# Performance work log

Hardware: AMD Instinct MI355X
Metric: run time of the kernel (lower is better)

## Reference

```python
import jax, jax.numpy as jnp
import numpy as np
from jax import lax

B, N, NPOINT, NSAMPLE = 8, 8192, 1024, 32
IN_CH = 64
MLP = [128, 128, 256]
EPS = 1e-5  # BatchNorm eps (inference mode with running stats)


def setup_inputs() -> dict:
    key = jax.random.key(0)
    ks = jax.random.split(key, 2 + len(MLP))
    inp = {
        "xyz": jax.random.normal(ks[0], (B, N, 3), jnp.float32),
        "feature": jax.random.normal(ks[1], (B, IN_CH, N), jnp.float32),
    }
    last = IN_CH
    for li, out in enumerate(MLP):
        k = jax.random.split(ks[2 + li], 3)
        inp[f"w{li}"] = jax.random.normal(k[0], (out, last), jnp.float32) / np.sqrt(last).astype(np.float32)
        inp[f"b{li}"] = jnp.zeros((out,), jnp.float32)
        inp[f"gamma{li}"] = jnp.ones((out,), jnp.float32)
        inp[f"beta{li}"] = jnp.zeros((out,), jnp.float32)
        inp[f"mean{li}"] = 0.1 * jax.random.normal(k[1], (out,), jnp.float32)
        inp[f"var{li}"] = 1.0 + 0.1 * jax.random.uniform(k[2], (out,), jnp.float32)
        last = out
    return inp


def furthest_point_sample(xyz, npoint):
    # xyz: [B, N, 3] -> idx [B, npoint] (sequential FPS via scan)
    Bn, Nn, _ = xyz.shape
    start = jnp.zeros((Bn,), jnp.int32)

    def step(carry, _):
        mind, last = carry
        p = jnp.take_along_axis(xyz, last[:, None, None], axis=1)  # [B,1,3]
        d = jnp.sum((xyz - p) ** 2, axis=-1)  # [B,N]
        mind = jnp.minimum(mind, d)
        nxt = jnp.argmax(mind, axis=-1).astype(jnp.int32)
        return (mind, nxt), nxt

    init = (jnp.full((Bn, Nn), 1e10, xyz.dtype), start)
    _, rest = lax.scan(step, init, None, length=npoint - 1)  # [npoint-1, B]
    return jnp.concatenate([start[None, :], rest], axis=0).T  # [B, npoint]


def k_neighbor_query(new_xyz, xyz, k):
    # squared distances via ||a||^2 + ||b||^2 - 2 a.b  (no [B,S,N,3] blowup)
    d = (jnp.sum(new_xyz ** 2, -1)[:, :, None]
         + jnp.sum(xyz ** 2, -1)[:, None, :]
         - 2.0 * jnp.einsum('bsc,bnc->bsn', new_xyz, xyz))  # [B,S,N]
    _, idx = lax.top_k(-d, k)  # k smallest distances
    return idx  # [B,S,k]


def _mlp_layers(x, params):
    # x: [B, Cin, S, k]; each layer: 1x1 conv -> BN (running stats) -> ReLU
    for (w, b, g, bt, m, v) in params:
        y = jnp.einsum('oi,bisk->bosk', w, x) + b[None, :, None, None]
        inv = (g / jnp.sqrt(v + EPS))[None, :, None, None]
        x = jax.nn.relu((y - m[None, :, None, None]) * inv + bt[None, :, None, None])
    return x


def reference(xyz, feature,
              w0, b0, gamma0, beta0, mean0, var0,
              w1, b1, gamma1, beta1, mean1, var1,
              w2, b2, gamma2, beta2, mean2, var2):
    idx = furthest_point_sample(xyz, NPOINT)                     # [B,S]
    new_xyz = jnp.take_along_axis(xyz, idx[:, :, None], axis=1)  # [B,S,3]
    nidx = k_neighbor_query(new_xyz, xyz, NSAMPLE)               # [B,S,k]
    # grouping_operation: gather neighbor features -> [B,D,S,k]
    grouped = jax.vmap(lambda f, i: f[:, i])(feature, nidx)
    params = [(w0, b0, gamma0, beta0, mean0, var0),
              (w1, b1, gamma1, beta1, mean1, var1),
              (w2, b2, gamma2, beta2, mean2, var2)]
    x = _mlp_layers(grouped, params)
    new_feature = jnp.max(x, axis=3)  # [B, D', S]
    return new_xyz, new_feature
```

## Files before the change

kernel.cpp:

```cpp
#include <hip/hip_runtime.h>
#include <hip/hip_bf16.h>
#include <math.h>

#define B_  8
#define N_  8192
#define S_  1024
#define K_  32
#define C0_ 64
#define NK  184
#define NM  64
#define NP_KNN 23
#define BINS 2048
#define CCAP 256

typedef __attribute__((ext_vector_type(8))) short short8;
typedef __attribute__((ext_vector_type(4))) float f32x4;
typedef __attribute__((ext_vector_type(2))) float f32x2;

#define WH_OFF    0
#define WL_OFF    114688
#define SC_OFF    229376
#define SH_OFF    231424
#define FT_OFF    233472
#define NIDX2_OFF 8622080
#define SLOT_OFF  10719232
#define FLAG_OFF  10915840
#define WL0E 0
#define WL1E 8192
#define WL2E 24576
#define FLAG_MAGIC(w) (0x5AB00000u | (unsigned)(w))

__device__ __forceinline__ void split_bf16(float x, unsigned short& h, unsigned short& l) {
    __hip_bfloat16 hb = __float2bfloat16(x);
    float hf = __bfloat162float(hb);
    __hip_bfloat16 lb = __float2bfloat16(x - hf);
    h = *(unsigned short*)&hb;
    l = *(unsigned short*)&lb;
}

__device__ __forceinline__ f32x4 mfma16(short8 a, short8 b, f32x4 c) {
    return __builtin_amdgcn_mfma_f32_16x16x32_bf16(a, b, c, 0, 0, 0);
}

template<int CTRL, int RMASK>
__device__ __forceinline__ unsigned long long dpp_max_step(unsigned long long k) {
    unsigned lo = (unsigned)k, hi = (unsigned)(k >> 32);
    unsigned tlo = (unsigned)__builtin_amdgcn_update_dpp(0, (int)lo, CTRL, RMASK, 0xF, false);
    unsigned thi = (unsigned)__builtin_amdgcn_update_dpp(0, (int)hi, CTRL, RMASK, 0xF, false);
    unsigned long long t = ((unsigned long long)thi << 32) | (unsigned long long)tlo;
    return (t > k) ? t : k;
}
__device__ __forceinline__ unsigned long long wave_max_u64(unsigned long long k) {
    k = dpp_max_step<0x111, 0xF>(k);
    k = dpp_max_step<0x112, 0xF>(k);
    k = dpp_max_step<0x114, 0xF>(k);
    k = dpp_max_step<0x118, 0xF>(k);
    k = dpp_max_step<0x142, 0xA>(k);
    k = dpp_max_step<0x143, 0xC>(k);
    return k;
}
__device__ __forceinline__ unsigned long long umax64(unsigned long long a, unsigned long long b) {
    return (a > b) ? a : b;
}

__device__ __forceinline__ void block_sync_lds() {
    asm volatile("" ::: "memory");
    __builtin_amdgcn_s_waitcnt(0xC07F);
    __builtin_amdgcn_s_barrier();
    asm volatile("" ::: "memory");
}

struct KnnSh {
    unsigned hist[2][BINS];
    unsigned long long cand[2][CCAP];
    unsigned long long kslots[2][2][4];
    int sel[2][K_];
    unsigned wpart[2][4];
    int sBin[2], sBelow[2];
    unsigned cnt_sel[2], cnt_cand[2];
    int fallback;
    float qpt[2][4];
};

template<int AF, int KC, bool LAST>
__device__ __forceinline__ void layer(
    const unsigned short* __restrict__ Xin, int rsi,
    unsigned short* __restrict__ Xout,
    const unsigned short* __restrict__ Wh, const unsigned short* __restrict__ Wl,
    const float* __restrict__ sc, const float* __restrict__ sh,
    float* __restrict__ outg, int wid, int ln15, int quad)
{
    const int K = KC * 32;
    f32x4 acc[AF][8];
    #pragma unroll
    for (int a = 0; a < AF; ++a)
        #pragma unroll
        for (int j = 0; j < 8; ++j) acc[a][j] = (f32x4){0.f, 0.f, 0.f, 0.f};

    #pragma unroll
    for (int kc = 0; kc < KC; ++kc) {
        const int k0 = kc * 32 + quad * 8;
        short8 bf[8];
        #pragma unroll
        for (int j = 0; j < 8; ++j)
            bf[j] = *(const short8*)(Xin + (j * 16 + ln15) * rsi + k0);
        #pragma unroll
        for (int a = 0; a < AF; ++a) {
            const int row = wid * (AF * 16) + a * 16 + ln15;
            short8 ah = *(const short8*)(Wh + (size_t)row * K + k0);
            short8 al = *(const short8*)(Wl + (size_t)row * K + k0);
            #pragma unroll
            for (int j = 0; j < 8; ++j) {
                acc[a][j] = mfma16(al, bf[j], acc[a][j]);
                acc[a][j] = mfma16(ah, bf[j], acc[a][j]);
            }
        }
    }
    #pragma unroll
    for (int a = 0; a < AF; ++a) {
        const int o4 = wid * (AF * 16) + a * 16 + quad * 4;
        f32x4 scv = *(const f32x4*)(sc + o4);
        f32x4 shv = *(const f32x4*)(sh + o4);
        if (LAST) {
            #pragma unroll
            for (int qq = 0; qq < 4; ++qq) {
                float m4[4];
                #pragma unroll
                for (int r = 0; r < 4; ++r) {
                    float v0 = fmaxf(acc[a][2 * qq][r]     * scv[r] + shv[r], 0.f);
                    float v1 = fmaxf(acc[a][2 * qq + 1][r] * scv[r] + shv[r], 0.f);
                    float mm = fmaxf(v0, v1);
                    mm = fmaxf(mm, __shfl_xor(mm, 1));
                    mm = fmaxf(mm, __shfl_xor(mm, 2));
                    mm = fmaxf(mm, __shfl_xor(mm, 4));
                    mm = fmaxf(mm, __shfl_xor(mm, 8));
                    m4[r] = mm;
                }
                if (ln15 == 0) {
                    #pragma unroll
                    for (int r = 0; r < 4; ++r)
                        outg[(size_t)(o4 + r) * S_ + qq] = m4[r];
                }
            }
        } else {
            #pragma unroll
            for (int j = 0; j < 8; ++j) {
                unsigned short pq[4];
                #pragma unroll
                for (int r = 0; r < 4; ++r) {
                    float v = fmaxf(acc[a][j][r] * scv[r] + shv[r], 0.f);
                    __hip_bfloat16 hb = __float2bfloat16(v);
                    pq[r] = *(unsigned short*)&hb;
                }
                *(unsigned long long*)(Xout + (j * 16 + ln15) * 136 + o4) = *(unsigned long long*)pq;
            }
        }
    }
}

__global__ __launch_bounds__(512, 2) void fused_kernel(
    const float* __restrict__ xyz, const float* __restrict__ feature,
    const float* __restrict__ w0, const float* __restrict__ w1, const float* __restrict__ w2,
    const float* __restrict__ b0, const float* __restrict__ g0, const float* __restrict__ be0,
    const float* __restrict__ m0, const float* __restrict__ v0,
    const float* __restrict__ b1, const float* __restrict__ g1, const float* __restrict__ be1,
    const float* __restrict__ m1, const float* __restrict__ v1,
    const float* __restrict__ b2, const float* __restrict__ g2, const float* __restrict__ be2,
    const float* __restrict__ m2, const float* __restrict__ v2,
    char* __restrict__ ws, float* __restrict__ out)
{
    __shared__ __align__(16) char smraw[131584];
    const int tid = threadIdx.x;
    const int bid = (int)blockIdx.x;

    if (bid < B_) {
        #pragma clang fp contract(off)
        const int b = bid;
        float4* xyzw = (float4*)smraw;
        unsigned long long* wredA = (unsigned long long*)(smraw + N_ * 16);
        unsigned long long* wredB = wredA + 8;
        unsigned long long* slots = (unsigned long long*)(ws + SLOT_OFF) + (size_t)b * S_ * 3;

        f32x2 px[8], py[8], pz[8], mind[8];
        const float* xb = xyz + (size_t)b * N_ * 3;
        #pragma unroll
        for (int j = 0; j < 8; ++j) {
            int n0 = (2 * j) * 512 + tid, n1 = n0 + 512;
            float x0 = xb[n0 * 3], y0 = xb[n0 * 3 + 1], z0 = xb[n0 * 3 + 2];
            float x1 = xb[n1 * 3], y1 = xb[n1 * 3 + 1], z1 = xb[n1 * 3 + 2];
            px[j] = (f32x2){x0, x1}; py[j] = (f32x2){y0, y1}; pz[j] = (f32x2){z0, z1};
            xyzw[n0] = make_float4(x0, y0, z0, 0.f);
            xyzw[n1] = make_float4(x1, y1, z1, 0.f);
            mind[j] = (f32x2){1e10f, 1e10f};
        }
        __syncthreads();

        float4 p0 = xyzw[0];
        float lx = p0.x, ly = p0.y, lz = p0.z;
        if (tid < 3) {
            float v = (tid == 0) ? lx : ((tid == 1) ? ly : lz);
            __hip_atomic_store(slots + tid, (unsigned long long)__float_as_uint(v),
                               __ATOMIC_RELAXED, __HIP_MEMORY_SCOPE_AGENT);
        }
        const int lane = tid & 63, wid = tid >> 6;

        for (int it = 1; it < S_; ++it) {
            f32x2 lx2 = (f32x2){lx, lx}, ly2 = (f32x2){ly, ly}, lz2 = (f32x2){lz, lz};
            float bv = -1.0f; int bj = 0;
            #pragma unroll
            for (int j = 0; j < 8; ++j) {
                f32x2 dx = px[j] - lx2;
                f32x2 dy = py[j] - ly2;
                f32x2 dz = pz[j] - lz2;
                f32x2 t = dx * dx;
                t = t + dy * dy;
                t = t + dz * dz;
                f32x2 mv = mind[j];
                float m0v = fminf(mv.x, t.x);
                float m1v = fminf(mv.y, t.y);
                mind[j] = (f32x2){m0v, m1v};
                if (m0v > bv) { bv = m0v; bj = 2 * j; }
                if (m1v > bv) { bv = m1v; bj = 2 * j + 1; }
            }
            unsigned long long key =
                ((unsigned long long)__float_as_uint(bv) << 32) |
                (unsigned long long)(0xFFFFFFFFu - (unsigned)(bj * 512 + tid));
            key = wave_max_u64(key);
            unsigned long long* wred = (it & 1) ? wredA : wredB;
            if (lane == 63) wred[wid] = key;
            block_sync_lds();
            unsigned long long g0v = umax64(wred[0], wred[1]);
            unsigned long long g1v = umax64(wred[2], wred[3]);
            unsigned long long g2v = umax64(wred[4], wred[5]);
            unsigned long long g3v = umax64(wred[6], wred[7]);
            unsigned long long g = umax64(umax64(g0v, g1v), umax64(g2v, g3v));
            int ns = (int)(0xFFFFFFFFu - (unsigned)(g & 0xFFFFFFFFull));
            float4 p = xyzw[ns];
            lx = p.x; ly = p.y; lz = p.z;
            if (tid < 3) {
                float v = (tid == 0) ? lx : ((tid == 1) ? ly : lz);
                __hip_atomic_store(slots + (size_t)it * 3 + tid,
                                   (((unsigned long long)(unsigned)it) << 32) | __float_as_uint(v),
                                   __ATOMIC_RELAXED, __HIP_MEMORY_SCOPE_AGENT);
            }
        }
        return;
    }

    if (bid < B_ + NK) {
        const int w = bid - B_;

        {
            unsigned short* th = (unsigned short*)smraw;
            for (int t = w; t < 1024; t += NK) {
                int bb = t >> 7, n0 = (t & 127) * 64;
                __syncthreads();
                {
                    int cg = tid >> 6, ln = tid & 63;
                    const float* fb = feature + (size_t)bb * C0_ * N_;
                    #pragma unroll
                    for (int i = 0; i < 8; ++i) {
                        int c = cg * 8 + i;
                        __hip_bfloat16 hb = __float2bfloat16(fb[(size_t)c * N_ + n0 + ln]);
                        th[ln * 72 + c] = *(unsigned short*)&hb;
                    }
                }
                __syncthreads();
                {
                    int n = tid >> 3, c0 = (tid & 7) * 8;
                    unsigned short* ft = (unsigned short*)(ws + FT_OFF) + ((size_t)(bb * N_ + n0 + n)) * C0_ + c0;
                    *(short8*)ft = *(const short8*)(th + n * 72 + c0);
                }
            }
        }
        if (w < 112) {
            int i = w * 512 + tid;
            float x;
            if (i < WL1E)      x = w0[i];
            else if (i < WL2E) x = w1[i - WL1E];
            else               x = w2[i - WL2E];
            unsigned short h, l;
            split_bf16(x, h, l);
            ((unsigned short*)(ws + WH_OFF))[i] = h;
            ((unsigned short*)(ws + WL_OFF))[i] = l;
        } else if (w == 112) {
            int o = tid;
            if (o < 512) {
                const float *bb_, *gg, *be_, *mm, *vv; int oo;
                if (o < 128)      { bb_ = b0; gg = g0; be_ = be0; mm = m0; vv = v0; oo = o; }
                else if (o < 256) { bb_ = b1; gg = g1; be_ = be1; mm = m1; vv = v1; oo = o - 128; }
                else              { bb_ = b2; gg = g2; be_ = be2; mm = m2; vv = v2; oo = o - 256; }
                float scv = gg[oo] / sqrtf(vv[oo] + 1e-5f);
                ((float*)(ws + SC_OFF))[o] = scv;
                ((float*)(ws + SH_OFF))[o] = (bb_[oo] - mm[oo]) * scv + be_[oo];
            }
        }
        __syncthreads();
        if (tid == 0)
            __hip_atomic_store((unsigned*)(ws + FLAG_OFF) + w, FLAG_MAGIC(w),
                               __ATOMIC_RELEASE, __HIP_MEMORY_SCOPE_AGENT);

        KnnSh* S = (KnnSh*)smraw;
        const int ht = tid & 255, half = tid >> 8;
        const int lane = tid & 63, widH = (tid >> 6) & 3;
        unsigned long long* nidx2 = (unsigned long long*)(ws + NIDX2_OFF);
        const unsigned long long* slots = (const unsigned long long*)(ws + SLOT_OFF);

        for (int p = 0; p < NP_KNN; ++p) {
            int qA = p * (NK * 2) + w * 2;
            int q = qA + half;
            bool active = q < B_ * S_;
            int qc = active ? q : (B_ * S_ - 1);
            int s = qc >> 3, bq = qc & 7;

            if (tid == 0) {
                #pragma unroll
                for (int h = 0; h < 2; ++h) {
                    int qq = qA + h;
                    if (qq >= B_ * S_) continue;
                    int ss = qq >> 3, bb = qq & 7;
                    const unsigned long long* sl = slots + ((size_t)bb * S_ + ss) * 3;
                    #pragma unroll
                    for (int c = 0; c < 3; ++c) {
                        unsigned long long v;
                        for (;;) {
                            v = __hip_atomic_load(sl + c, __ATOMIC_RELAXED, __HIP_MEMORY_SCOPE_AGENT);
                            if ((int)(v >> 32) == ss) break;
                            __builtin_amdgcn_s_sleep(8);
                        }
                        S->qpt[h][c] = __uint_as_float((unsigned)v);
                    }
                }
            }
            __syncthreads();

            if (active && ht < 3) out[(size_t)(bq * S_ + s) * 3 + ht] = S->qpt[half][ht];

            #pragma unroll
            for (int i = 0; i < BINS / 256; ++i) S->hist[half][ht + i * 256] = 0;
            if (ht == 0) { S->cnt_sel[half] = 0; S->cnt_cand[half] = 0; if (tid == 0) S->fallback = 0; }

            float qx = S->qpt[half][0], qy = S->qpt[half][1], qz = S->qpt[half][2];
            float sa = __fadd_rn(__fadd_rn(__fmul_rn(qx, qx), __fmul_rn(qy, qy)), __fmul_rn(qz, qz));

            unsigned key[32];
            const float* base = xyz + (size_t)bq * N_ * 3;
            #pragma unroll
            for (int i = 0; i < 32; ++i) {
                int n = i * 256 + ht;
                float x = base[n * 3], y = base[n * 3 + 1], z = base[n * 3 + 2];
                float sb  = __fadd_rn(__fadd_rn(__fmul_rn(x, x), __fmul_rn(y, y)), __fmul_rn(z, z));
                float dot = __fadd_rn(__fadd_rn(__fmul_rn(qx, x), __fmul_rn(qy, y)), __fmul_rn(qz, z));
                float d   = __fsub_rn(__fadd_rn(sa, sb), __fmul_rn(2.0f, dot));
                unsigned u = __float_as_uint(d);
                key[i] = u ^ (unsigned)(((int)u >> 31) | (int)0x80000000);
            }
            __syncthreads();
            if (active) {
                #pragma unroll
                for (int i = 0; i < 32; ++i) atomicAdd(&S->hist[half][key[i] >> 21], 1u);
            }
            __syncthreads();

            unsigned h8[8], lsum = 0;
            #pragma unroll
            for (int i = 0; i < 8; ++i) { h8[i] = S->hist[half][ht * 8 + i]; lsum += h8[i]; }
            unsigned inc = lsum;
            #pragma unroll
            for (int off = 1; off < 64; off <<= 1) {
                unsigned o = __shfl_up(inc, off);
                if (lane >= off) inc += o;
            }
            if (lane == 63) S->wpart[half][widH] = inc;
            __syncthreads();
            unsigned basec = 0;
            #pragma unroll
            for (int w4 = 0; w4 < 4; ++w4) if (w4 < widH) basec += S->wpart[half][w4];
            unsigned excl = basec + inc - lsum;
            if (active && excl < (unsigned)K_ && excl + lsum >= (unsigned)K_) {
                unsigned c = excl;
                #pragma unroll
                for (int i = 0; i < 8; ++i) {
                    if (c < (unsigned)K_ && c + h8[i] >= (unsigned)K_) { S->sBin[half] = ht * 8 + i; S->sBelow[half] = (int)c; }
                    c += h8[i];
                }
            }
            __syncthreads();
            const unsigned Bbin = (unsigned)S->sBin[half];
            const int below = S->sBelow[half];

            if (active) {
                #pragma unroll
                for (int i = 0; i < 32; ++i) {
                    unsigned bin = key[i] >> 21;
                    int n = i * 256 + ht;
                    if (bin < Bbin) {
                        unsigned pp = atomicAdd(&S->cnt_sel[half], 1u);
                        if (pp < (unsigned)K_) S->sel[half][pp] = n;
                    } else if (bin == Bbin) {
                        unsigned pp = atomicAdd(&S->cnt_cand[half], 1u);
                        if (pp < CCAP) S->cand[half][pp] = ((unsigned long long)key[i] << 32) | (unsigned)n;
                    }
                }
            }
            __syncthreads();
            int m = (int)S->cnt_cand[half];
            if (active && ht == 0 && m > CCAP) S->fallback = 1;
            __syncthreads();

            if (!S->fallback) {
                if (widH == 0) {
                    int mtake = active ? (K_ - below) : 0;
                    if (mtake < 0) mtake = 0; if (mtake > K_) mtake = K_;
                    int mm = active ? m : 0;
                    unsigned long long v[4];
                    #pragma unroll
                    for (int j = 0; j < 4; ++j) {
                        int pp = lane + j * 64;
                        v[j] = (pp < mm) ? S->cand[half][pp] : ~0ull;
                    }
                    for (int r = 0; r < mtake; ++r) {
                        unsigned long long loc = v[0];
                        #pragma unroll
                        for (int j = 1; j < 4; ++j) if (v[j] < loc) loc = v[j];
                        unsigned long long g = loc;
                        #pragma unroll
                        for (int off = 1; off < 64; off <<= 1) {
                            unsigned long long o = __shfl_xor(g, off);
                            if (o < g) g = o;
                        }
                        #pragma unroll
                        for (int j = 0; j < 4; ++j) if (v[j] == g) v[j] = ~0ull;
                        if (lane == 0) S->sel[half][below + r] = (int)(unsigned)(g & 0xFFFFFFFFull);
                    }
                }
                __syncthreads();
            } else {
                unsigned bk = 0xFFFFFFFFu; int bi = 0;
                #pragma unroll
                for (int i = 0; i < 32; ++i) if (key[i] < bk) { bk = key[i]; bi = i; }
                for (int r = 0; r < K_; ++r) {
                    unsigned long long pk = ((unsigned long long)bk << 32) | (unsigned)(bi * 256 + ht);
                    #pragma unroll
                    for (int off = 1; off < 64; off <<= 1) {
                        unsigned long long o = __shfl_xor(pk, off);
                        if (o < pk) pk = o;
                    }
                    if (lane == 0) S->kslots[half][r & 1][widH] = pk;
                    __syncthreads();
                    unsigned long long g = S->kslots[half][r & 1][0];
                    #pragma unroll
                    for (int w4 = 1; w4 < 4; ++w4) { unsigned long long o = S->kslots[half][r & 1][w4]; if (o < g) g = o; }
                    int wn = (int)(unsigned)(g & 0xFFFFFFFFull);
                    if (ht == 0) S->sel[half][r] = wn;
                    if ((wn & 255) == ht) {
                        int iw = wn >> 8;
                        #pragma unroll
                        for (int ii = 0; ii < 32; ++ii) if (ii == iw) key[ii] = 0xFFFFFFFFu;
                        bk = 0xFFFFFFFFu; bi = 0;
                        #pragma unroll
                        for (int ii = 0; ii < 32; ++ii) if (key[ii] < bk) { bk = key[ii]; bi = ii; }
                    }
                }
                __syncthreads();
            }
            if (active && ht < K_)
                __hip_atomic_store(nidx2 + (size_t)q * K_ + ht,
                                   (((unsigned long long)(unsigned)q) << 32) | (unsigned)S->sel[half][ht],
                                   __ATOMIC_RELAXED, __HIP_MEMORY_SCOPE_AGENT);
            __syncthreads();
        }
        return;
    }

    {
        const int m = bid - B_ - NK;
        const int ht = tid & 255;
        const int lane = tid & 63, widH = (tid >> 6) & 3;
        const int ln15 = lane & 15, quad = lane >> 4;

        unsigned short* XA = (unsigned short*)smraw;
        unsigned short* XB = (unsigned short*)(smraw + 34816);
        int* nid = (int*)(smraw + 69632);

        {
            volatile unsigned* fl = (volatile unsigned*)(ws + FLAG_OFF);
            if (tid < NK) {
                while (__hip_atomic_load((const unsigned*)(ws + FLAG_OFF) + tid,
                                         __ATOMIC_RELAXED, __HIP_MEMORY_SCOPE_AGENT) != FLAG_MAGIC(tid))
                    __builtin_amdgcn_s_sleep(16);
            }
            (void)fl;
            __syncthreads();
            if (tid == 0) __threadfence();
            __syncthreads();
        }

        const unsigned short* FT = (const unsigned short*)(ws + FT_OFF);
        const unsigned short* Wh = (const unsigned short*)(ws + WH_OFF);
        const unsigned short* Wl = (const unsigned short*)(ws + WL_OFF);
        const float* sc = (const float*)(ws + SC_OFF);
        const float* sh = (const float*)(ws + SH_OFF);
        const unsigned long long* nidx2 = (const unsigned long long*)(ws + NIDX2_OFF);

        for (int t = m; t < 2048; t += NM) {
            int s4 = t >> 3, bq = t & 7, s0 = s4 * 4;
            if (ht < 128) {
                int qi = ht >> 5, k = ht & 31;
                int q = bq + 8 * (s0 + qi);
                const unsigned long long* ptr = nidx2 + (size_t)q * K_ + k;
                unsigned long long v;
                for (;;) {
                    v = __hip_atomic_load(ptr, __ATOMIC_RELAXED, __HIP_MEMORY_SCOPE_AGENT);
                    if ((int)(v >> 32) == q) break;
                    __builtin_amdgcn_s_sleep(8);
                }
                nid[ht] = (int)(unsigned)(v & 0xFFFFFFFFull);
            }
            __syncthreads();

            #pragma unroll
            for (int it = 0; it < 4; ++it) {
                int idx = it * 256 + ht;
                int row = idx >> 3, slot = idx & 7;
                short8 v = *(const short8*)(FT + ((size_t)(bq * N_ + nid[row])) * C0_ + slot * 8);
                *(short8*)(XA + row * 72 + slot * 8) = v;
            }
            __syncthreads();

            layer<2, 2, false>(XA, 72,  XB, Wh + WL0E, Wl + WL0E, sc,       sh,       nullptr, widH, ln15, quad);
            __syncthreads();
            layer<2, 4, false>(XB, 136, XA, Wh + WL1E, Wl + WL1E, sc + 128, sh + 128, nullptr, widH, ln15, quad);
            __syncthreads();
            float* outg = out + (size_t)B_ * S_ * 3 + (size_t)bq * 256 * S_ + s0;
            layer<4, 4, true>(XA, 136, nullptr, Wh + WL2E, Wl + WL2E, sc + 256, sh + 256, outg, widH, ln15, quad);
            __syncthreads();
        }
    }
}

extern "C" void kernel_launch(void* const* d_in, const int* in_sizes, int n_in,
                              void* d_out, int out_size, void* d_ws, size_t ws_size,
                              hipStream_t stream) {
    const float* xyz     = (const float*)d_in[0];
    const float* feature = (const float*)d_in[1];
    const float* w0 = (const float*)d_in[2];
    const float* b0 = (const float*)d_in[3];
    const float* g0 = (const float*)d_in[4];
    const float* be0 = (const float*)d_in[5];
    const float* m0 = (const float*)d_in[6];
    const float* v0 = (const float*)d_in[7];
    const float* w1 = (const float*)d_in[8];
    const float* b1 = (const float*)d_in[9];
    const float* g1 = (const float*)d_in[10];
    const float* be1 = (const float*)d_in[11];
    const float* m1 = (const float*)d_in[12];
    const float* v1 = (const float*)d_in[13];
    const float* w2 = (const float*)d_in[14];
    const float* b2 = (const float*)d_in[15];
    const float* g2 = (const float*)d_in[16];
    const float* be2 = (const float*)d_in[17];
    const float* m2 = (const float*)d_in[18];
    const float* v2 = (const float*)d_in[19];

    float* out = (float*)d_out;
    char*  ws  = (char*)d_ws;

    void* kargs[] = {
        (void*)&xyz, (void*)&feature, (void*)&w0, (void*)&w1, (void*)&w2,
        (void*)&b0, (void*)&g0, (void*)&be0, (void*)&m0, (void*)&v0,
        (void*)&b1, (void*)&g1, (void*)&be1, (void*)&m1, (void*)&v1,
        (void*)&b2, (void*)&g2, (void*)&be2, (void*)&m2, (void*)&v2,
        (void*)&ws, (void*)&out };
    hipError_t ce = hipLaunchCooperativeKernel((void*)fused_kernel,
                                               dim3(B_ + NK + NM), dim3(512), kargs, 0, stream);
    if (ce != hipSuccess) {
        fused_kernel<<<B_ + NK + NM, 512, 0, stream>>>(xyz, feature, w0, w1, w2,
            b0, g0, be0, m0, v0, b1, g1, be1, m1, v1, b2, g2, be2, m2, v2, ws, out);
    }
}
```

Baseline: 1.256 ms.

## Split furthest-point sampling across four blocks per batch with global exchange

Furthest-point sampling for each batch now runs on four cooperating blocks instead of one. Each block owns 2048 points, reduces a local argmax, and publishes its key and coordinates to a global exchange buffer tagged with the iteration number. It then spin-waits on the other three blocks' entries to agree on the next point. This cuts per-iteration arithmetic per block and frees register pressure, which matters because FPS is the long sequential critical path. The cost is a cross-block global-memory handshake on every one of the 1023 iterations. Block counts for the KNN and MLP roles are rebalanced (168/56, NP_KNN 25) to fit the extra FPS blocks.

```diff
diff --git a/kernel.cpp b/kernel.cpp
--- a/kernel.cpp
+++ b/kernel.cpp
@@ -7,15 +7,15 @@
 #define S_  1024
 #define K_  32
 #define C0_ 64
-#define NK  184
-#define NM  64
-#define NP_KNN 23
+#define NF  32
+#define NK  168
+#define NM  56
+#define NP_KNN 25
 #define BINS 2048
 #define CCAP 256
 
 typedef __attribute__((ext_vector_type(8))) short short8;
 typedef __attribute__((ext_vector_type(4))) float f32x4;
-typedef __attribute__((ext_vector_type(2))) float f32x2;
 
 #define WH_OFF    0
 #define WL_OFF    114688
@@ -25,6 +25,7 @@
 #define NIDX2_OFF 8622080
 #define SLOT_OFF  10719232
 #define FLAG_OFF  10915840
+#define EX_OFF    10917888
 #define WL0E 0
 #define WL1E 8192
 #define WL2E 24576
@@ -173,82 +174,125 @@
     const int tid = threadIdx.x;
     const int bid = (int)blockIdx.x;
 
-    if (bid < B_) {
-        #pragma clang fp contract(off)
-        const int b = bid;
-        float4* xyzw = (float4*)smraw;
-        unsigned long long* wredA = (unsigned long long*)(smraw + N_ * 16);
+    if (bid < NF) {
+        const int b = bid & 7, sub = bid >> 3;
+        float4* xl = (float4*)smraw;
+        unsigned long long* wredA = (unsigned long long*)(smraw + 32768);
         unsigned long long* wredB = wredA + 8;
+        unsigned* exb = (unsigned*)(smraw + 33024);
+        float* bc = (float*)(smraw + 33152);
         unsigned long long* slots = (unsigned long long*)(ws + SLOT_OFF) + (size_t)b * S_ * 3;
-
-        f32x2 px[8], py[8], pz[8], mind[8];
-        const float* xb = xyz + (size_t)b * N_ * 3;
+        unsigned long long* ex = (unsigned long long*)(ws + EX_OFF);
+
+        float px[4], py[4], pz[4], mind[4]; unsigned nin[4];
+        const float* xb = xyz + ((size_t)b * N_ + sub * 2048) * 3;
         #pragma unroll
-        for (int j = 0; j < 8; ++j) {
-            int n0 = (2 * j) * 512 + tid, n1 = n0 + 512;
-            float x0 = xb[n0 * 3], y0 = xb[n0 * 3 + 1], z0 = xb[n0 * 3 + 2];
-            float x1 = xb[n1 * 3], y1 = xb[n1 * 3 + 1], z1 = xb[n1 * 3 + 2];
-            px[j] = (f32x2){x0, x1}; py[j] = (f32x2){y0, y1}; pz[j] = (f32x2){z0, z1};
-            xyzw[n0] = make_float4(x0, y0, z0, 0.f);
-            xyzw[n1] = make_float4(x1, y1, z1, 0.f);
-            mind[j] = (f32x2){1e10f, 1e10f};
-        }
-        __syncthreads();
-
-        float4 p0 = xyzw[0];
-        float lx = p0.x, ly = p0.y, lz = p0.z;
-        if (tid < 3) {
+        for (int j = 0; j < 4; ++j) {
+            int idx = j * 512 + tid;
+            float x = xb[idx * 3], y = xb[idx * 3 + 1], z = xb[idx * 3 + 2];
+            px[j] = x; py[j] = y; pz[j] = z;
+            xl[idx] = make_float4(x, y, z, 0.f);
+            mind[j] = 1e10f;
+            nin[j] = 0xFFFFFFFFu - (unsigned)(sub * 2048 + idx);
+        }
+        float lx = xyz[(size_t)b * N_ * 3 + 0];
+        float ly = xyz[(size_t)b * N_ * 3 + 1];
+        float lz = xyz[(size_t)b * N_ * 3 + 2];
+        if (sub == 0 && tid < 3) {
             float v = (tid == 0) ? lx : ((tid == 1) ? ly : lz);
             __hip_atomic_store(slots + tid, (unsigned long long)__float_as_uint(v),
                                __ATOMIC_RELAXED, __HIP_MEMORY_SCOPE_AGENT);
         }
+        __syncthreads();
         const int lane = tid & 63, wid = tid >> 6;
 
         for (int it = 1; it < S_; ++it) {
-            f32x2 lx2 = (f32x2){lx, lx}, ly2 = (f32x2){ly, ly}, lz2 = (f32x2){lz, lz};
-            float bv = -1.0f; int bj = 0;
-            #pragma unroll
-            for (int j = 0; j < 8; ++j) {
-                f32x2 dx = px[j] - lx2;
-                f32x2 dy = py[j] - ly2;
-                f32x2 dz = pz[j] - lz2;
-                f32x2 t = dx * dx;
-                t = t + dy * dy;
-                t = t + dz * dz;
-                f32x2 mv = mind[j];
-                float m0v = fminf(mv.x, t.x);
-                float m1v = fminf(mv.y, t.y);
-                mind[j] = (f32x2){m0v, m1v};
-                if (m0v > bv) { bv = m0v; bj = 2 * j; }
-                if (m1v > bv) { bv = m1v; bj = 2 * j + 1; }
-            }
-            unsigned long long key =
-                ((unsigned long long)__float_as_uint(bv) << 32) |
-                (unsigned long long)(0xFFFFFFFFu - (unsigned)(bj * 512 + tid));
-            key = wave_max_u64(key);
+            unsigned long long kk;
+            {
+                unsigned long long k0, k1, k2, k3;
+                float dx, dy, dz, dd, mj;
+                dx = __fsub_rn(px[0], lx); dy = __fsub_rn(py[0], ly); dz = __fsub_rn(pz[0], lz);
+                dd = __fadd_rn(__fadd_rn(__fmul_rn(dx, dx), __fmul_rn(dy, dy)), __fmul_rn(dz, dz));
+                mj = fminf(mind[0], dd); mind[0] = mj;
+                k0 = ((unsigned long long)__float_as_uint(mj) << 32) | (unsigned long long)nin[0];
+                dx = __fsub_rn(px[1], lx); dy = __fsub_rn(py[1], ly); dz = __fsub_rn(pz[1], lz);
+                dd = __fadd_rn(__fadd_rn(__fmul_rn(dx, dx), __fmul_rn(dy, dy)), __fmul_rn(dz, dz));
+                mj = fminf(mind[1], dd); mind[1] = mj;
+                k1 = ((unsigned long long)__float_as_uint(mj) << 32) | (unsigned long long)nin[1];
+                dx = __fsub_rn(px[2], lx); dy = __fsub_rn(py[2], ly); dz = __fsub_rn(pz[2], lz);
+                dd = __fadd_rn(__fadd_rn(__fmul_rn(dx, dx), __fmul_rn(dy, dy)), __fmul_rn(dz, dz));
+                mj = fminf(mind[2], dd); mind[2] = mj;
+                k2 = ((unsigned long long)__float_as_uint(mj) << 32) | (unsigned long long)nin[2];
+                dx = __fsub_rn(px[3], lx); dy = __fsub_rn(py[3], ly); dz = __fsub_rn(pz[3], lz);
+                dd = __fadd_rn(__fadd_rn(__fmul_rn(dx, dx), __fmul_rn(dy, dy)), __fmul_rn(dz, dz));
+                mj = fminf(mind[3], dd); mind[3] = mj;
+                k3 = ((unsigned long long)__float_as_uint(mj) << 32) | (unsigned long long)nin[3];
+                kk = umax64(umax64(k0, k1), umax64(k2, k3));
+            }
+            kk = wave_max_u64(kk);
             unsigned long long* wred = (it & 1) ? wredA : wredB;
-            if (lane == 63) wred[wid] = key;
+            if (lane == 63) wred[wid] = kk;
             block_sync_lds();
-            unsigned long long g0v = umax64(wred[0], wred[1]);
-            unsigned long long g1v = umax64(wred[2], wred[3]);
-            unsigned long long g2v = umax64(wred[4], wred[5]);
-            unsigned long long g3v = umax64(wred[6], wred[7]);
-            unsigned long long g = umax64(umax64(g0v, g1v), umax64(g2v, g3v));
-            int ns = (int)(0xFFFFFFFFu - (unsigned)(g & 0xFFFFFFFFull));
-            float4 p = xyzw[ns];
-            lx = p.x; ly = p.y; lz = p.z;
-            if (tid < 3) {
-                float v = (tid == 0) ? lx : ((tid == 1) ? ly : lz);
-                __hip_atomic_store(slots + (size_t)it * 3 + tid,
-                                   (((unsigned long long)(unsigned)it) << 32) | __float_as_uint(v),
-                                   __ATOMIC_RELAXED, __HIP_MEMORY_SCOPE_AGENT);
-            }
+            if (wid == 0) {
+                unsigned long long g0v = umax64(wred[0], wred[1]);
+                unsigned long long g1v = umax64(wred[2], wred[3]);
+                unsigned long long g2v = umax64(wred[4], wred[5]);
+                unsigned long long g3v = umax64(wred[6], wred[7]);
+                unsigned long long g = umax64(umax64(g0v, g1v), umax64(g2v, g3v));
+                unsigned ghi = (unsigned)(g >> 32), glo = (unsigned)g;
+                int nsl = (int)(0xFFFFFFFFu - glo) - sub * 2048;
+                float4 wp = xl[nsl];
+                unsigned long long tg = ((unsigned long long)(unsigned)it) << 32;
+                size_t exbase = ((size_t)((b << 10) | it)) * 20;
+                if (lane < 5) {
+                    unsigned pay = (lane == 0) ? ghi : (lane == 1) ? glo :
+                                   (lane == 2) ? __float_as_uint(wp.x) :
+                                   (lane == 3) ? __float_as_uint(wp.y) : __float_as_uint(wp.z);
+                    __hip_atomic_store(ex + exbase + sub * 5 + lane, tg | pay,
+                                       __ATOMIC_RELAXED, __HIP_MEMORY_SCOPE_AGENT);
+                }
+                if (lane >= 16 && lane < 31) {
+                    int j2 = lane - 16, p = j2 / 5, c = j2 - p * 5;
+                    int psub = p + (p >= sub ? 1 : 0);
+                    const unsigned long long* pa = ex + exbase + psub * 5 + c;
+                    unsigned long long v;
+                    for (;;) {
+                        v = __hip_atomic_load(pa, __ATOMIC_RELAXED, __HIP_MEMORY_SCOPE_AGENT);
+                        if ((unsigned)(v >> 32) == (unsigned)it) break;
+                        __builtin_amdgcn_s_sleep(1);
+                    }
+                    exb[j2] = (unsigned)v;
+                }
+                asm volatile("" ::: "memory");
+                __builtin_amdgcn_s_waitcnt(0xC07F);
+                asm volatile("" ::: "memory");
+                unsigned long long bk = g;
+                float wx = wp.x, wy = wp.y, wz = wp.z;
+                #pragma unroll
+                for (int p = 0; p < 3; ++p) {
+                    unsigned long long kp = ((unsigned long long)exb[p * 5] << 32) | exb[p * 5 + 1];
+                    if (kp > bk) {
+                        bk = kp;
+                        wx = __uint_as_float(exb[p * 5 + 2]);
+                        wy = __uint_as_float(exb[p * 5 + 3]);
+                        wz = __uint_as_float(exb[p * 5 + 4]);
+                    }
+                }
+                if (lane == 0) { bc[0] = wx; bc[1] = wy; bc[2] = wz; }
+                if (sub == 0 && lane < 3) {
+                    float v = (lane == 0) ? wx : ((lane == 1) ? wy : wz);
+                    __hip_atomic_store(slots + (size_t)it * 3 + lane, tg | __float_as_uint(v),
+                                       __ATOMIC_RELAXED, __HIP_MEMORY_SCOPE_AGENT);
+                }
+            }
+            block_sync_lds();
+            lx = bc[0]; ly = bc[1]; lz = bc[2];
         }
         return;
     }
 
-    if (bid < B_ + NK) {
-        const int w = bid - B_;
+    if (bid < NF + NK) {
+        const int w = bid - NF;
 
         {
             unsigned short* th = (unsigned short*)smraw;
@@ -474,7 +518,7 @@
     }
 
     {
-        const int m = bid - B_ - NK;
+        const int m = bid - NF - NK;
         const int ht = tid & 255;
         const int lane = tid & 63, widH = (tid >> 6) & 3;
         const int ln15 = lane & 15, quad = lane >> 4;
@@ -484,13 +528,11 @@
         int* nid = (int*)(smraw + 69632);
 
         {
-            volatile unsigned* fl = (volatile unsigned*)(ws + FLAG_OFF);
             if (tid < NK) {
                 while (__hip_atomic_load((const unsigned*)(ws + FLAG_OFF) + tid,
                                          __ATOMIC_RELAXED, __HIP_MEMORY_SCOPE_AGENT) != FLAG_MAGIC(tid))
                     __builtin_amdgcn_s_sleep(16);
             }
-            (void)fl;
             __syncthreads();
             if (tid == 0) __threadfence();
             __syncthreads();
@@ -573,9 +615,9 @@
         (void*)&b2, (void*)&g2, (void*)&be2, (void*)&m2, (void*)&v2,
         (void*)&ws, (void*)&out };
     hipError_t ce = hipLaunchCooperativeKernel((void*)fused_kernel,
-                                               dim3(B_ + NK + NM), dim3(512), kargs, 0, stream);
+                                               dim3(NF + NK + NM), dim3(512), kargs, 0, stream);
     if (ce != hipSuccess) {
-        fused_kernel<<<B_ + NK + NM, 512, 0, stream>>>(xyz, feature, w0, w1, w2,
+        fused_kernel<<<NF + NK + NM, 512, 0, stream>>>(xyz, feature, w0, w1, w2,
             b0, g0, be0, m0, v0, b1, g1, be1, m1, v1, b2, g2, be2, m2, v2, ws, out);
     }
 }
```

After: 1.546 ms. 1.23x slower.
